# Kernel tuning notes

Measured on AMD Instinct MI355X. Metric: run time of the kernel, lower is better.

Reference implementation:

```python
import jax, jax.numpy as jnp
import numpy as np
import math

HIDDEN = 1024
HEADS = 16
HEAD_DIM = HIDDEN // HEADS
B, S = 2, 2048


def _xavier(key, shape):
    fan_in, fan_out = shape[1], shape[0]
    limit = math.sqrt(6.0 / (fan_in + fan_out))
    return jax.random.uniform(key, shape, jnp.float32, -limit, limit)


def setup_inputs() -> dict:
    key = jax.random.key(0)
    ks = jax.random.split(key, 5)
    x = jax.random.normal(ks[0], (B, S, HIDDEN), jnp.float32)
    # torch Linear stores weight as [out, in]; y = x @ W.T + b
    Wq = _xavier(ks[1], (HIDDEN, HIDDEN))
    Wk = _xavier(ks[2], (HIDDEN, HIDDEN))
    Wv = _xavier(ks[3], (HIDDEN, HIDDEN))
    Wo = _xavier(ks[4], (HIDDEN, HIDDEN))
    bq = jnp.zeros((HIDDEN,), jnp.float32)
    bk = jnp.zeros((HIDDEN,), jnp.float32)
    bv = jnp.zeros((HIDDEN,), jnp.float32)
    bo = jnp.zeros((HIDDEN,), jnp.float32)
    return {"x": x, "Wq": Wq, "bq": bq, "Wk": Wk, "bk": bk,
            "Wv": Wv, "bv": bv, "Wo": Wo, "bo": bo}


def reference(x, Wq, bq, Wk, bk, Wv, bv, Wo, bo):
    b, s, d = x.shape
    h, hd = HEADS, HEAD_DIM
    q = (x @ Wq.T + bq).reshape(b, s, h, hd).transpose(0, 2, 1, 3)  # [b,h,s,hd]
    k = (x @ Wk.T + bk).reshape(b, s, h, hd).transpose(0, 2, 1, 3)
    v = (x @ Wv.T + bv).reshape(b, s, h, hd).transpose(0, 2, 1, 3)
    scores = jnp.einsum('bhqd,bhkd->bhqk', q, k) / math.sqrt(hd)
    causal = jnp.tril(jnp.ones((s, s), bool))
    scores = jnp.where(causal, scores, -jnp.inf)
    attn = jax.nn.softmax(scores, axis=-1)
    out = jnp.einsum('bhqk,bhkd->bhqd', attn, v)  # [b,h,s,hd]
    out = out.transpose(0, 2, 1, 3).reshape(b, s, d)
    return out @ Wo.T + bo
```

## Files before the change

### kernel.cpp

```cpp
#include <hip/hip_runtime.h>
#include <hip/hip_bf16.h>


typedef __hip_bfloat16 bf16;
typedef __attribute__((ext_vector_type(8))) short short8;
typedef __attribute__((ext_vector_type(4))) short short4v;
typedef __attribute__((ext_vector_type(4))) float f32x4;

#define MFMA16(a, b, c) __builtin_amdgcn_mfma_f32_16x16x32_bf16((a), (b), (c), 0, 0, 0)

__device__ __forceinline__ void load_lds16(const void* g, void* l) {
  __builtin_amdgcn_global_load_lds(
      (const __attribute__((address_space(1))) void*)g,
      (__attribute__((address_space(3))) void*)l, 16, 0, 0);
}

#define QSCALE 0.18033688f

__global__ __launch_bounds__(256) void cvt_kernel(
    const float* __restrict__ x, const float* __restrict__ wq,
    const float* __restrict__ wk, const float* __restrict__ wv,
    const float* __restrict__ wo, bf16* __restrict__ xb,
    bf16* __restrict__ wcat) {
  const int bx = blockIdx.x;
  const float* src;
  bf16* dst;
  int ib;
  if (bx < 4096) { src = x; dst = xb; ib = bx; }
  else {
    const int wseg = (bx - 4096) >> 10;
    ib = (bx - 4096) & 1023;
    src = wseg == 0 ? wq : wseg == 1 ? wk : wseg == 2 ? wv : wo;
    dst = wcat + (size_t)wseg * 1048576;
  }
  const int i = (ib * 256 + threadIdx.x) * 4;
  const float4 v = *(const float4*)(src + i);
  short4v p;
  *(__hip_bfloat162*)&p = __float22bfloat162_rn(float2{v.x, v.y});
  *((__hip_bfloat162*)&p + 1) = __float22bfloat162_rn(float2{v.z, v.w});
  *(short4v*)(dst + i) = p;
}

__global__ __launch_bounds__(256) void qkv_kernel(
    const bf16* __restrict__ x, const bf16* __restrict__ Wcat,
    const float* __restrict__ bq, const float* __restrict__ bk,
    const float* __restrict__ bv, bf16* __restrict__ Qb,
    bf16* __restrict__ Kb, bf16* __restrict__ Vtg) {
  constexpr int K = 1024;
  __shared__ bf16 As[128 * 64];
  __shared__ bf16 Bs[128 * 64];
  const int t = threadIdx.x;
  const int lane = t & 63, w = t >> 6;
  const int quad = lane >> 4, r = lane & 15;
  const int m0 = blockIdx.y * 128;
  const int ncol = blockIdx.x * 128;
  const int seg = ncol >> 10;
  const int n0 = ncol & 1023;
  const int wm = w >> 1, wn = w & 1;

  f32x4 acc[4][4] = {};

  for (int k0 = 0; k0 < K; k0 += 64) {
    __syncthreads();
#pragma unroll
    for (int p = 0; p < 4; ++p) {
      const int c = p * 256 + w * 64 + lane;
      const int row = c >> 3;
      const int scb = (c & 7) ^ (row & 7);
      load_lds16(x + (size_t)(m0 + row) * K + k0 + scb * 8, As + c * 8);
    }
#pragma unroll
    for (int p = 0; p < 4; ++p) {
      const int c = p * 256 + w * 64 + lane;
      const int row = c >> 3;
      const int scb = (c & 7) ^ (row & 7);
      load_lds16(Wcat + (size_t)(ncol + row) * K + k0 + scb * 8, Bs + c * 8);
    }
    __syncthreads();
    short8 af[4][2], bfr[4][2];
#pragma unroll
    for (int ks = 0; ks < 2; ++ks) {
#pragma unroll
      for (int i = 0; i < 4; ++i) {
        const int ra = wm * 64 + i * 16 + r;
        af[i][ks] = *(const short8*)(As + ra * 64 +
                                     (((ks * 4 + quad) ^ (ra & 7)) * 8));
        const int rb = wn * 64 + i * 16 + r;
        bfr[i][ks] = *(const short8*)(Bs + rb * 64 +
                                      (((ks * 4 + quad) ^ (rb & 7)) * 8));
      }
    }
#pragma unroll
    for (int ks = 0; ks < 2; ++ks)
#pragma unroll
      for (int i = 0; i < 4; ++i)
#pragma unroll
        for (int j = 0; j < 4; ++j)
          acc[i][j] = MFMA16(af[i][ks], bfr[j][ks], acc[i][j]);
  }

  const float* bias = seg == 0 ? bq : seg == 1 ? bk : bv;
  const float scale = seg == 0 ? QSCALE : 1.0f;
  bf16* dst01 = seg == 0 ? Qb : Kb;
#pragma unroll
  for (int i = 0; i < 4; ++i) {
    const int m = m0 + wm * 64 + i * 16 + quad * 4;
#pragma unroll
    for (int j = 0; j < 4; ++j) {
      const int nn = n0 + wn * 64 + j * 16 + r;
      const float bv_ = bias[nn];
      if (seg == 2) {
        short4v pk;
        *(__hip_bfloat162*)&pk = __float22bfloat162_rn(
            float2{acc[i][j][0] + bv_, acc[i][j][1] + bv_});
        *((__hip_bfloat162*)&pk + 1) = __float22bfloat162_rn(
            float2{acc[i][j][2] + bv_, acc[i][j][3] + bv_});
        *(short4v*)(Vtg + (size_t)nn * 4096 + m) = pk;
      } else {
#pragma unroll
        for (int g = 0; g < 4; ++g)
          dst01[(size_t)(m + g) * 1024 + nn] =
              __float2bfloat16((acc[i][j][g] + bv_) * scale);
      }
    }
  }
}

__global__ __launch_bounds__(256) void proj_kernel(const bf16* __restrict__ X,
                                                   const bf16* __restrict__ W,
                                                   const float* __restrict__ bias,
                                                   float* __restrict__ Y) {
  constexpr int K = 1024, N = 1024;
  __shared__ bf16 As[64 * 64];
  __shared__ bf16 Bs[128 * 64];
  const int t = threadIdx.x;
  const int lane = t & 63, w = t >> 6;
  const int quad = lane >> 4, r = lane & 15;
  const int m0 = blockIdx.y * 64, n0 = blockIdx.x * 128;
  const int wm = w >> 1, wn = w & 1;

  f32x4 acc[2][4] = {};

  for (int k0 = 0; k0 < K; k0 += 64) {
    __syncthreads();
#pragma unroll
    for (int p = 0; p < 2; ++p) {
      const int c = p * 256 + w * 64 + lane;
      const int row = c >> 3;
      const int scb = (c & 7) ^ (row & 7);
      load_lds16(X + (size_t)(m0 + row) * K + k0 + scb * 8, As + c * 8);
    }
#pragma unroll
    for (int p = 0; p < 4; ++p) {
      const int c = p * 256 + w * 64 + lane;
      const int row = c >> 3;
      const int scb = (c & 7) ^ (row & 7);
      load_lds16(W + (size_t)(n0 + row) * K + k0 + scb * 8, Bs + c * 8);
    }
    __syncthreads();
    short8 af[2][2], bfr[4][2];
#pragma unroll
    for (int ks = 0; ks < 2; ++ks) {
#pragma unroll
      for (int i = 0; i < 2; ++i) {
        const int ra = wm * 32 + i * 16 + r;
        af[i][ks] = *(const short8*)(As + ra * 64 +
                                     (((ks * 4 + quad) ^ (ra & 7)) * 8));
      }
#pragma unroll
      for (int j = 0; j < 4; ++j) {
        const int rb = wn * 64 + j * 16 + r;
        bfr[j][ks] = *(const short8*)(Bs + rb * 64 +
                                      (((ks * 4 + quad) ^ (rb & 7)) * 8));
      }
    }
#pragma unroll
    for (int ks = 0; ks < 2; ++ks)
#pragma unroll
      for (int i = 0; i < 2; ++i)
#pragma unroll
        for (int j = 0; j < 4; ++j)
          acc[i][j] = MFMA16(af[i][ks], bfr[j][ks], acc[i][j]);
  }
#pragma unroll
  for (int i = 0; i < 2; ++i) {
    const int m = m0 + wm * 32 + i * 16 + quad * 4;
#pragma unroll
    for (int j = 0; j < 4; ++j) {
      const int n = n0 + wn * 64 + j * 16 + r;
      const float bv = bias[n];
#pragma unroll
      for (int g = 0; g < 4; ++g)
        Y[(size_t)(m + g) * N + n] = acc[i][j][g] + bv;
    }
  }
}

__global__ __launch_bounds__(256) void attn_kernel(const bf16* __restrict__ Qb,
                                                   const bf16* __restrict__ Kb,
                                                   const bf16* __restrict__ Vtg,
                                                   bf16* __restrict__ Ob) {
  const int pair = blockIdx.x, h = blockIdx.y, b = blockIdx.z;
  const int t = threadIdx.x;
  const int lane = t & 63, w = t >> 6;
  const int quad = lane >> 4, r = lane & 15;

  __shared__ bf16 Ks[128 * 64];
  __shared__ bf16 Vt[64 * 128];
  __shared__ bf16 Pl[4][16 * 128];

  int rowK[4], scbK[4], rowV[4], scbV[4];
  bf16 *klds[4], *vlds[4];
#pragma unroll
  for (int p = 0; p < 4; ++p) {
    const int c = p * 256 + w * 64 + lane;
    rowK[p] = c >> 3;  scbK[p] = (c & 7) ^ (rowK[p] & 7);
    rowV[p] = c >> 4;  scbV[p] = (c & 15) ^ (rowV[p] & 15);
    klds[p] = Ks + c * 8;
    vlds[p] = Vt + c * 8;
  }

#pragma unroll 1
  for (int sel = 0; sel < 2; ++sel) {
    const int j = sel ? (31 - pair) : pair;
    const int qrow = j * 64 + w * 16 + r;

    short8 qf[2];
#pragma unroll
    for (int ks = 0; ks < 2; ++ks)
      qf[ks] = *(const short8*)(Qb + (size_t)(b * 2048 + qrow) * 1024 + h * 64 +
                                ks * 32 + quad * 8);

    const bf16 *kp[4], *vp[4];
#pragma unroll
    for (int p = 0; p < 4; ++p) {
      kp[p] = Kb + (size_t)(b * 2048 + rowK[p]) * 1024 + h * 64 + scbK[p] * 8;
      vp[p] = Vtg + (size_t)(h * 64 + rowV[p]) * 4096 + b * 2048 + scbV[p] * 8;
    }

    f32x4 o[4] = {};
    float lsum = 0.f;

    const int nkt = j / 2 + 1;
    for (int kt = 0; kt < nkt; ++kt) {
      const int k0 = kt * 128;
      __syncthreads();
#pragma unroll
      for (int p = 0; p < 4; ++p) load_lds16(kp[p], klds[p]);
#pragma unroll
      for (int p = 0; p < 4; ++p) load_lds16(vp[p], vlds[p]);
#pragma unroll
      for (int p = 0; p < 4; ++p) { kp[p] += 128 * 1024; vp[p] += 128; }
      __syncthreads();

      f32x4 st[8] = {};
#pragma unroll
      for (int ks = 0; ks < 2; ++ks) {
        short8 kf[8];
#pragma unroll
        for (int mt = 0; mt < 8; ++mt) {
          const int key = mt * 16 + r;
          kf[mt] = *(const short8*)(Ks + key * 64 +
                                    (((ks * 4 + quad) ^ (key & 7)) * 8));
        }
#pragma unroll
        for (int mt = 0; mt < 8; ++mt) st[mt] = MFMA16(kf[mt], qf[ks], st[mt]);
      }

      if (kt == nkt - 1) {
#pragma unroll
        for (int mt = 0; mt < 8; ++mt)
#pragma unroll
          for (int g = 0; g < 4; ++g) {
            const int key = k0 + mt * 16 + quad * 4 + g;
            if (key > qrow) st[mt][g] = -1e30f;
          }
      }

#pragma unroll
      for (int mt = 0; mt < 8; ++mt) {
        const float p0 = exp2f(st[mt][0]), p1 = exp2f(st[mt][1]);
        const float p2 = exp2f(st[mt][2]), p3 = exp2f(st[mt][3]);
        lsum += (p0 + p1) + (p2 + p3);
        short4v pk;
        *(__hip_bfloat162*)&pk = __float22bfloat162_rn(float2{p0, p1});
        *((__hip_bfloat162*)&pk + 1) = __float22bfloat162_rn(float2{p2, p3});
        const int key8 = mt * 2 + (quad >> 1);
        const int off = r * 128 + ((key8 ^ (r & 15)) * 8) + (quad & 1) * 4;
        *(short4v*)(&Pl[w][off]) = pk;
      }

      asm volatile("s_waitcnt lgkmcnt(0)" ::: "memory");

#pragma unroll
      for (int ks = 0; ks < 4; ++ks) {
        short8 vf[4], pf;
#pragma unroll
        for (int mt = 0; mt < 4; ++mt) {
          const int d = mt * 16 + r;
          vf[mt] = *(const short8*)(Vt + d * 128 +
                                    (((ks * 4 + quad) ^ (d & 15)) * 8));
        }
        pf = *(const short8*)(Pl[w] + r * 128 +
                              (((ks * 4 + quad) ^ (r & 15)) * 8));
#pragma unroll
        for (int mt = 0; mt < 4; ++mt) o[mt] = MFMA16(vf[mt], pf, o[mt]);
      }
    }

    lsum += __shfl_xor(lsum, 16);
    lsum += __shfl_xor(lsum, 32);
    const float inv = 1.f / lsum;

#pragma unroll
    for (int mt = 0; mt < 4; ++mt) {
      const int d0 = mt * 16 + quad * 4;
      short4v pk;
      *(__hip_bfloat162*)&pk = __float22bfloat162_rn(
          float2{o[mt][0] * inv, o[mt][1] * inv});
      *((__hip_bfloat162*)&pk + 1) = __float22bfloat162_rn(
          float2{o[mt][2] * inv, o[mt][3] * inv});
      *(short4v*)(Ob + (size_t)(b * 2048 + qrow) * 1024 + h * 64 + d0) = pk;
    }
  }
}

extern "C" void kernel_launch(void* const* d_in, const int* in_sizes, int n_in,
                              void* d_out, int out_size, void* d_ws, size_t ws_size,
                              hipStream_t stream) {
  const float* x  = (const float*)d_in[0];
  const float* Wq = (const float*)d_in[1];
  const float* bq = (const float*)d_in[2];
  const float* Wk = (const float*)d_in[3];
  const float* bk = (const float*)d_in[4];
  const float* Wv = (const float*)d_in[5];
  const float* bv = (const float*)d_in[6];
  const float* Wo = (const float*)d_in[7];
  const float* bo = (const float*)d_in[8];
  float* out = (float*)d_out;

  bf16* xb   = (bf16*)d_ws;
  bf16* wcat = xb + (size_t)4096 * 1024;
  bf16* wob  = wcat + (size_t)3 * 1024 * 1024;
  bf16* Qb   = wcat + (size_t)4 * 1024 * 1024;
  bf16* Kb   = Qb  + (size_t)4096 * 1024;
  bf16* Vtg  = Kb  + (size_t)4096 * 1024;
  bf16* Ob   = Vtg + (size_t)4096 * 1024;
  const size_t need = ((size_t)4096 * 1024 * 5 + (size_t)1024 * 1024 * 4) * 2;
  if (ws_size < need) return;

  cvt_kernel<<<8192, 256, 0, stream>>>(x, Wq, Wk, Wv, Wo, xb, wcat);
  qkv_kernel<<<dim3(24, 32), 256, 0, stream>>>(xb, wcat, bq, bk, bv,
                                               Qb, Kb, Vtg);
  attn_kernel<<<dim3(16, 16, 2), 256, 0, stream>>>(Qb, Kb, Vtg, Ob);
  proj_kernel<<<dim3(8, 64), 256, 0, stream>>>(Ob, wob, bo, out);
}
```

Baseline: 189.9 us.

## Process both paired query blocks in one pass sharing K/V tile loads

The attention kernel previously looped over the low and high query blocks of a pair one after the other, reloading K/V tiles for each. It now walks the key tiles once for the high block and, while the low block is still active, reuses the same K/V tiles in LDS to compute the low block's scores and PV products too. This cuts global-to-LDS traffic and barriers for the shared prefix. In exchange it doubles the P buffer in LDS and keeps two output accumulators live, which raises register and LDS pressure and may lower occupancy.

Result: faster. 184.6 us (-2.8%).

```diff
diff --git a/kernel.cpp b/kernel.cpp
--- a/kernel.cpp
+++ b/kernel.cpp
@@ -207,52 +207,53 @@
 
   __shared__ bf16 Ks[128 * 64];
   __shared__ bf16 Vt[64 * 128];
-  __shared__ bf16 Pl[4][16 * 128];
-
-  int rowK[4], scbK[4], rowV[4], scbV[4];
+  __shared__ bf16 Pl[4][2][16 * 128];
+
+  const bf16 *kp[4], *vp[4];
   bf16 *klds[4], *vlds[4];
 #pragma unroll
   for (int p = 0; p < 4; ++p) {
     const int c = p * 256 + w * 64 + lane;
-    rowK[p] = c >> 3;  scbK[p] = (c & 7) ^ (rowK[p] & 7);
-    rowV[p] = c >> 4;  scbV[p] = (c & 15) ^ (rowV[p] & 15);
+    const int rowK = c >> 3, scbK = (c & 7) ^ (rowK & 7);
+    const int rowV = c >> 4, scbV = (c & 15) ^ (rowV & 15);
     klds[p] = Ks + c * 8;
     vlds[p] = Vt + c * 8;
-  }
-
-#pragma unroll 1
-  for (int sel = 0; sel < 2; ++sel) {
-    const int j = sel ? (31 - pair) : pair;
-    const int qrow = j * 64 + w * 16 + r;
-
-    short8 qf[2];
-#pragma unroll
-    for (int ks = 0; ks < 2; ++ks)
-      qf[ks] = *(const short8*)(Qb + (size_t)(b * 2048 + qrow) * 1024 + h * 64 +
-                                ks * 32 + quad * 8);
-
-    const bf16 *kp[4], *vp[4];
-#pragma unroll
-    for (int p = 0; p < 4; ++p) {
-      kp[p] = Kb + (size_t)(b * 2048 + rowK[p]) * 1024 + h * 64 + scbK[p] * 8;
-      vp[p] = Vtg + (size_t)(h * 64 + rowV[p]) * 4096 + b * 2048 + scbV[p] * 8;
-    }
-
-    f32x4 o[4] = {};
-    float lsum = 0.f;
-
-    const int nkt = j / 2 + 1;
-    for (int kt = 0; kt < nkt; ++kt) {
-      const int k0 = kt * 128;
-      __syncthreads();
-#pragma unroll
-      for (int p = 0; p < 4; ++p) load_lds16(kp[p], klds[p]);
-#pragma unroll
-      for (int p = 0; p < 4; ++p) load_lds16(vp[p], vlds[p]);
-#pragma unroll
-      for (int p = 0; p < 4; ++p) { kp[p] += 128 * 1024; vp[p] += 128; }
-      __syncthreads();
-
+    kp[p] = Kb + (size_t)(b * 2048 + rowK) * 1024 + h * 64 + scbK * 8;
+    vp[p] = Vtg + (size_t)(h * 64 + rowV) * 4096 + b * 2048 + scbV * 8;
+  }
+
+  const int jlo = pair, jhi = 31 - pair;
+  const int nkt_lo = jlo / 2 + 1, nkt_hi = jhi / 2 + 1;
+  const int qrow_lo = jlo * 64 + w * 16 + r;
+  const int qrow_hi = jhi * 64 + w * 16 + r;
+
+  short8 qfl[2], qfh[2];
+#pragma unroll
+  for (int ks = 0; ks < 2; ++ks) {
+    qfl[ks] = *(const short8*)(Qb + (size_t)(b * 2048 + qrow_lo) * 1024 +
+                               h * 64 + ks * 32 + quad * 8);
+    qfh[ks] = *(const short8*)(Qb + (size_t)(b * 2048 + qrow_hi) * 1024 +
+                               h * 64 + ks * 32 + quad * 8);
+  }
+
+  f32x4 oh[4] = {}, ol[4] = {};
+  float lsh = 0.f, lsl = 0.f;
+
+  for (int kt = 0; kt < nkt_hi; ++kt) {
+    const int k0 = kt * 128;
+    __syncthreads();
+#pragma unroll
+    for (int p = 0; p < 4; ++p) load_lds16(kp[p], klds[p]);
+#pragma unroll
+    for (int p = 0; p < 4; ++p) load_lds16(vp[p], vlds[p]);
+#pragma unroll
+    for (int p = 0; p < 4; ++p) { kp[p] += 128 * 1024; vp[p] += 128; }
+    __syncthreads();
+
+    const bool lo_act = (kt < nkt_lo);
+
+    auto s_phase = [&](const short8* qf, int qrow, bool mask, int qi,
+                       float& lsum) {
       f32x4 st[8] = {};
 #pragma unroll
       for (int ks = 0; ks < 2; ++ks) {
@@ -266,8 +267,7 @@
 #pragma unroll
         for (int mt = 0; mt < 8; ++mt) st[mt] = MFMA16(kf[mt], qf[ks], st[mt]);
       }
-
-      if (kt == nkt - 1) {
+      if (mask) {
 #pragma unroll
         for (int mt = 0; mt < 8; ++mt)
 #pragma unroll
@@ -276,7 +276,6 @@
             if (key > qrow) st[mt][g] = -1e30f;
           }
       }
-
 #pragma unroll
       for (int mt = 0; mt < 8; ++mt) {
         const float p0 = exp2f(st[mt][0]), p1 = exp2f(st[mt][1]);
@@ -287,41 +286,56 @@
         *((__hip_bfloat162*)&pk + 1) = __float22bfloat162_rn(float2{p2, p3});
         const int key8 = mt * 2 + (quad >> 1);
         const int off = r * 128 + ((key8 ^ (r & 15)) * 8) + (quad & 1) * 4;
-        *(short4v*)(&Pl[w][off]) = pk;
-      }
-
-      asm volatile("s_waitcnt lgkmcnt(0)" ::: "memory");
-
-#pragma unroll
-      for (int ks = 0; ks < 4; ++ks) {
-        short8 vf[4], pf;
-#pragma unroll
-        for (int mt = 0; mt < 4; ++mt) {
-          const int d = mt * 16 + r;
-          vf[mt] = *(const short8*)(Vt + d * 128 +
-                                    (((ks * 4 + quad) ^ (d & 15)) * 8));
-        }
-        pf = *(const short8*)(Pl[w] + r * 128 +
-                              (((ks * 4 + quad) ^ (r & 15)) * 8));
-#pragma unroll
-        for (int mt = 0; mt < 4; ++mt) o[mt] = MFMA16(vf[mt], pf, o[mt]);
-      }
-    }
-
-    lsum += __shfl_xor(lsum, 16);
-    lsum += __shfl_xor(lsum, 32);
-    const float inv = 1.f / lsum;
-
-#pragma unroll
-    for (int mt = 0; mt < 4; ++mt) {
-      const int d0 = mt * 16 + quad * 4;
-      short4v pk;
-      *(__hip_bfloat162*)&pk = __float22bfloat162_rn(
-          float2{o[mt][0] * inv, o[mt][1] * inv});
-      *((__hip_bfloat162*)&pk + 1) = __float22bfloat162_rn(
-          float2{o[mt][2] * inv, o[mt][3] * inv});
-      *(short4v*)(Ob + (size_t)(b * 2048 + qrow) * 1024 + h * 64 + d0) = pk;
-    }
+        *(short4v*)(&Pl[w][qi][off]) = pk;
+      }
+    };
+
+    s_phase(qfh, qrow_hi, kt == nkt_hi - 1, 0, lsh);
+    if (lo_act) s_phase(qfl, qrow_lo, kt == nkt_lo - 1, 1, lsl);
+
+    asm volatile("s_waitcnt lgkmcnt(0)" ::: "memory");
+
+#pragma unroll
+    for (int ks = 0; ks < 4; ++ks) {
+      short8 vf[4];
+#pragma unroll
+      for (int mt = 0; mt < 4; ++mt) {
+        const int d = mt * 16 + r;
+        vf[mt] = *(const short8*)(Vt + d * 128 +
+                                  (((ks * 4 + quad) ^ (d & 15)) * 8));
+      }
+      const int poff = r * 128 + (((ks * 4 + quad) ^ (r & 15)) * 8);
+      const short8 pfh = *(const short8*)(Pl[w][0] + poff);
+#pragma unroll
+      for (int mt = 0; mt < 4; ++mt) oh[mt] = MFMA16(vf[mt], pfh, oh[mt]);
+      if (lo_act) {
+        const short8 pfl = *(const short8*)(Pl[w][1] + poff);
+#pragma unroll
+        for (int mt = 0; mt < 4; ++mt) ol[mt] = MFMA16(vf[mt], pfl, ol[mt]);
+      }
+    }
+  }
+
+  lsh += __shfl_xor(lsh, 16);
+  lsh += __shfl_xor(lsh, 32);
+  lsl += __shfl_xor(lsl, 16);
+  lsl += __shfl_xor(lsl, 32);
+  const float invh = 1.f / lsh, invl = 1.f / lsl;
+
+#pragma unroll
+  for (int mt = 0; mt < 4; ++mt) {
+    const int d0 = mt * 16 + quad * 4;
+    short4v ph, pl2;
+    *(__hip_bfloat162*)&ph = __float22bfloat162_rn(
+        float2{oh[mt][0] * invh, oh[mt][1] * invh});
+    *((__hip_bfloat162*)&ph + 1) = __float22bfloat162_rn(
+        float2{oh[mt][2] * invh, oh[mt][3] * invh});
+    *(short4v*)(Ob + (size_t)(b * 2048 + qrow_hi) * 1024 + h * 64 + d0) = ph;
+    *(__hip_bfloat162*)&pl2 = __float22bfloat162_rn(
+        float2{ol[mt][0] * invl, ol[mt][1] * invl});
+    *((__hip_bfloat162*)&pl2 + 1) = __float22bfloat162_rn(
+        float2{ol[mt][2] * invl, ol[mt][3] * invl});
+    *(short4v*)(Ob + (size_t)(b * 2048 + qrow_lo) * 1024 + h * 64 + d0) = pl2;
   }
 }
 
```
